# Performance work log

Measured on AMD Instinct MI355X. Metric: run time of the kernel, lower is better.

The kernel has to match this reference:

```python
import jax, jax.numpy as jnp
import numpy as np

B, T, E, D = 8, 2048, 1024, 128  # batch, seq, embedding_dim, head_dim


def setup_inputs() -> dict:
    key = jax.random.key(0)
    ks = jax.random.split(key, 7)
    s = 1.0 / np.sqrt(E)  # torch Linear default init scale
    return {
        "x": jax.random.normal(ks[0], (B, T, E), dtype=jnp.float32),
        "Wq": jax.random.uniform(ks[1], (E, D), jnp.float32, -s, s),
        "bq": jax.random.uniform(ks[2], (D,), jnp.float32, -s, s),
        "Wk": jax.random.uniform(ks[3], (E, D), jnp.float32, -s, s),
        "bk": jax.random.uniform(ks[4], (D,), jnp.float32, -s, s),
        "Wv": jax.random.uniform(ks[5], (E, D), jnp.float32, -s, s),
        "bv": jax.random.uniform(ks[6], (D,), jnp.float32, -s, s),
        "mask": 1,
    }


def reference(x, Wq, bq, Wk, bk, Wv, bv, mask):
    # Q/K/V projections: [B,T,E] @ [E,D] -> [B,T,D]
    q = x @ Wq + bq
    k = x @ Wk + bk
    v = x @ Wv + bv
    d_k = q.shape[-1]
    # scores: [B,T,T]
    scores = jnp.einsum("btd,bsd->bts", q, k) / jnp.sqrt(jnp.float32(d_k))
    if mask:  # causal masked_fill with -inf (static python flag)
        causal = jnp.tril(jnp.ones((q.shape[1], q.shape[1]), dtype=bool))
        scores = jnp.where(causal[None, :, :], scores, -jnp.inf)
    att = jax.nn.softmax(scores, axis=-1)
    # dropout p=0.0 (inference) -> identity
    return jnp.einsum("bts,bsd->btd", att, v)
```

## Files before the change

### kernel.cpp

```cpp
#include <hip/hip_runtime.h>
#include <hip/hip_bf16.h>

#define BSZ  8
#define TSEQ 2048
#define EDIM 1024
#define DDIM 128
#define MROWS (BSZ * TSEQ)
#define NQT  (TSEQ / 64)

typedef __attribute__((ext_vector_type(8))) __bf16 bf16x8;
typedef __attribute__((ext_vector_type(4))) __bf16 bf16x4;
typedef __attribute__((ext_vector_type(2))) __bf16 bf16x2;
typedef __attribute__((ext_vector_type(4))) float f32x4;

#define GLOAD_LDS(G, L) \
    __builtin_amdgcn_global_load_lds( \
        (const __attribute__((address_space(1))) void*)(G), \
        (__attribute__((address_space(3))) void*)(L), 16, 0, 0)

__global__ __launch_bounds__(256) void wt_kernel(
    const float* __restrict__ Wq, const float* __restrict__ Wk,
    const float* __restrict__ Wv, __bf16* __restrict__ wt)
{
    const float* W = (blockIdx.y == 0) ? Wq : (blockIdx.y == 1) ? Wk : Wv;
    __bf16* o = wt + (size_t)blockIdx.y * DDIM * EDIM;
    const int k0 = blockIdx.x * 64;
    __shared__ __align__(16) __bf16 t[64][140];
    const int tid = threadIdx.x;
    #pragma unroll
    for (int i = 0; i < 8; ++i) {
        int idx = tid + i * 256;
        int k = idx >> 5, c4 = idx & 31;
        float4 v = *(const float4*)&W[(size_t)(k0 + k) * DDIM + c4 * 4];
        bf16x4 b4;
        b4[0] = (__bf16)v.x; b4[1] = (__bf16)v.y; b4[2] = (__bf16)v.z; b4[3] = (__bf16)v.w;
        *(bf16x4*)&t[k][c4 * 4] = b4;
    }
    __syncthreads();
    #pragma unroll
    for (int i = 0; i < 4; ++i) {
        int idx = tid + i * 256;
        int n = idx >> 3, c8 = idx & 7;
        bf16x8 r;
        #pragma unroll
        for (int u = 0; u < 8; ++u) r[u] = t[c8 * 8 + u][n];
        *(bf16x8*)&o[(size_t)n * EDIM + k0 + c8 * 8] = r;
    }
}

#define A_LDS_BYTES 16384
#define B_LDS_BYTES 24576
#define BUF_BYTES   (A_LDS_BYTES + B_LDS_BYTES)

__global__ __launch_bounds__(256, 2) void qkv_fused_kernel(
    const float* __restrict__ x, const __bf16* __restrict__ wt,
    const float* __restrict__ bq, const float* __restrict__ bk,
    const float* __restrict__ bv,
    __bf16* __restrict__ qo, __bf16* __restrict__ ko, __bf16* __restrict__ vto)
{
    const int bid = blockIdx.x;
    const int xcd = bid & 7;
    const int nt  = (bid >> 3) & 1;
    const int mt  = (bid >> 4) * 8 + xcd;
    const int m0  = mt * 64;

    __shared__ __align__(16) char lds[2 * BUF_BYTES];

    const int tid  = threadIdx.x;
    const int lane = tid & 63;
    const int wv   = tid >> 6;
    const int wr   = wv >> 1, wc = wv & 1;
    const int cl   = lane & 15, gr = lane >> 4;

    f32x4 acc[2][6] = {};

    const float* asrc[4];
    int adst[4];
    #pragma unroll
    for (int i = 0; i < 4; ++i) {
        const int row  = i * 16 + (tid >> 4);
        const int lcol = ((tid & 15) * 16) ^ ((row & 7) << 4);
        asrc[i] = x + (size_t)(m0 + row) * EDIM + (lcol >> 2);
        adst[i] = i * 4096 + tid * 16;
    }
    const __bf16* bsrc[6];
    int bdst[6];
    #pragma unroll
    for (int i = 0; i < 6; ++i) {
        const int row  = i * 32 + (tid >> 3);
        const int lcol = ((tid & 7) * 16) ^ ((row & 7) << 4);
        bsrc[i] = wt + (size_t)(nt * 192 + row) * EDIM + (lcol >> 1);
        bdst[i] = A_LDS_BYTES + i * 4096 + tid * 16;
    }

    const int sw = (cl & 7) << 4;

#define STAGE(BUF, K0) do {                                                   \
    _Pragma("unroll")                                                         \
    for (int i = 0; i < 4; ++i)                                               \
        GLOAD_LDS(asrc[i] + (K0), lds + (BUF) * BUF_BYTES + adst[i]);         \
    _Pragma("unroll")                                                         \
    for (int i = 0; i < 6; ++i)                                               \
        GLOAD_LDS(bsrc[i] + (K0), lds + (BUF) * BUF_BYTES + bdst[i]);         \
  } while (0)

#define COMPUTE(BUF) do {                                                     \
    const char* base_ = lds + (BUF) * BUF_BYTES;                              \
    _Pragma("unroll")                                                         \
    for (int ks = 0; ks < 2; ++ks) {                                          \
        bf16x8 af[2], bfr[6];                                                 \
        _Pragma("unroll")                                                     \
        for (int mi = 0; mi < 2; ++mi) {                                      \
            const int ab = (wr * 32 + mi * 16 + cl) * 256 + ks * 128;         \
            f32x4 lo = *(const f32x4*)(base_ + ab + ((gr * 32)      ^ sw));   \
            f32x4 hi = *(const f32x4*)(base_ + ab + ((gr * 32 + 16) ^ sw));   \
            bf16x8 t;                                                         \
            t[0] = (__bf16)lo[0]; t[1] = (__bf16)lo[1];                       \
            t[2] = (__bf16)lo[2]; t[3] = (__bf16)lo[3];                       \
            t[4] = (__bf16)hi[0]; t[5] = (__bf16)hi[1];                       \
            t[6] = (__bf16)hi[2]; t[7] = (__bf16)hi[3];                       \
            af[mi] = t;                                                       \
        }                                                                     \
        _Pragma("unroll")                                                     \
        for (int ni = 0; ni < 6; ++ni) {                                      \
            const int off = A_LDS_BYTES + (wc * 96 + ni * 16 + cl) * 128      \
                          + ((ks * 64 + gr * 16) ^ sw);                       \
            bfr[ni] = *(const bf16x8*)(base_ + off);                          \
        }                                                                     \
        _Pragma("unroll")                                                     \
        for (int mi = 0; mi < 2; ++mi)                                        \
            _Pragma("unroll")                                                 \
            for (int ni = 0; ni < 6; ++ni)                                    \
                acc[mi][ni] = __builtin_amdgcn_mfma_f32_16x16x32_bf16(        \
                    af[mi], bfr[ni], acc[mi][ni], 0, 0, 0);                   \
    }                                                                         \
  } while (0)

    STAGE(0, 0);
    __syncthreads();

    #pragma unroll 1
    for (int k0 = 0; k0 < EDIM; k0 += 128) {
        STAGE(1, k0 + 64);
        COMPUTE(0);
        __syncthreads();
        if (k0 + 128 < EDIM) STAGE(0, k0 + 128);
        COMPUTE(1);
        __syncthreads();
    }
#undef STAGE
#undef COMPUTE

    const float qsc = 0.08838834764831845f;
    #pragma unroll
    for (int ni = 0; ni < 6; ++ni) {
        const int nbase = nt * 192 + wc * 96 + ni * 16;
        const int which = nbase >> 7;
        const int d     = (nbase & 127) + cl;
        const float* bias = (which == 0) ? bq : (which == 1) ? bk : bv;
        const float bb = bias[d];
        const float sc = (which == 0) ? qsc : 1.0f;
        #pragma unroll
        for (int mi = 0; mi < 2; ++mi) {
            const int row = m0 + wr * 32 + mi * 16 + gr * 4;
            if (which == 2) {
                bf16x4 p;
                #pragma unroll
                for (int r = 0; r < 4; ++r) p[r] = (__bf16)(acc[mi][ni][r] + bb);
                *(bf16x4*)&vto[(size_t)d * MROWS + row] = p;
            } else {
                __bf16* o = (which == 0) ? qo : ko;
                #pragma unroll
                for (int r = 0; r < 4; ++r)
                    o[(size_t)(row + r) * DDIM + d] = (__bf16)((acc[mi][ni][r] + bb) * sc);
            }
        }
    }
}

__global__ __launch_bounds__(256, 3) void attn_partial_kernel(
    const __bf16* __restrict__ Q, const __bf16* __restrict__ K,
    const __bf16* __restrict__ Vt,
    __bf16* __restrict__ partO, float* __restrict__ partM, float* __restrict__ partL,
    int PL, int NP)
{
    const int bid = blockIdx.x;
    const int b   = blockIdx.y;

    int g = 0, rem = bid;
    for (;;) {
        const int np_g = (g + 1 + PL - 1) / PL;
        if (rem < np_g) break;
        rem -= np_g; ++g;
    }
    const int qt = g, p = rem;
    const int tiles = qt + 1;
    const int np = (tiles + PL - 1) / PL;
    const int lb = tiles / np, ex = tiles % np;
    const int mylen = lb + (p < ex);
    const int start = p * lb + min(p, ex);
    const int kv_lo = start * 64;
    const int kv_hi = kv_lo + mylen * 64;

    __shared__ __align__(16) __bf16 k_lds[64][136];
    __shared__ __align__(16) __bf16 v_lds[128][72];
    __shared__ __align__(16) __bf16 p_lds[4][16][72];

    const int tid  = threadIdx.x;
    const int lane = tid & 63;
    const int w    = tid >> 6;
    const int cl   = lane & 15, gr = lane >> 4;

    const int qrow = qt * 64 + w * 16;
    const size_t bT = (size_t)b * TSEQ;

    bf16x8 qf[4];
    const __bf16* qbase = Q + (bT + qrow + cl) * DDIM;
    #pragma unroll
    for (int ks = 0; ks < 4; ++ks)
        qf[ks] = *(const bf16x8*)&qbase[ks * 32 + gr * 8];

    f32x4 acc[8] = {};
    float m1 = -__builtin_inff();
    float l1 = 0.f;

    bf16x8 rk[4], rv[4];
#define LOAD_TILE(KV0) do {                                                   \
    _Pragma("unroll")                                                         \
    for (int i = 0; i < 4; ++i) {                                             \
        int idx = tid + i * 256;                                              \
        rk[i] = *(const bf16x8*)&K[(bT + (KV0) + (idx >> 4)) * DDIM + (idx & 15) * 8]; } \
    _Pragma("unroll")                                                         \
    for (int i = 0; i < 4; ++i) {                                             \
        int idx = tid + i * 256;                                              \
        rv[i] = *(const bf16x8*)&Vt[(size_t)(idx >> 3) * MROWS + bT + (KV0) + (idx & 7) * 8]; } \
  } while (0)

    LOAD_TILE(kv_lo);

    for (int kv0 = kv_lo; kv0 < kv_hi; kv0 += 64) {
        #pragma unroll
        for (int i = 0; i < 4; ++i) {
            int idx = tid + i * 256;
            *(bf16x8*)&k_lds[idx >> 4][(idx & 15) * 8] = rk[i];
        }
        #pragma unroll
        for (int i = 0; i < 4; ++i) {
            int idx = tid + i * 256;
            *(bf16x8*)&v_lds[idx >> 3][(idx & 7) * 8] = rv[i];
        }
        __syncthreads();

        if (kv0 + 64 < kv_hi) LOAD_TILE(kv0 + 64);

        f32x4 s[4] = {};
        #pragma unroll
        for (int ks = 0; ks < 4; ++ks) {
            #pragma unroll
            for (int st = 0; st < 4; ++st) {
                bf16x8 kf = *(const bf16x8*)&k_lds[st * 16 + cl][ks * 32 + gr * 8];
                s[st] = __builtin_amdgcn_mfma_f32_16x16x32_bf16(kf, qf[ks], s[st], 0, 0, 0);
            }
        }

        if (kv0 + 63 > qrow) {
            const int kvb = kv0 + gr * 4 - qrow - cl;
            #pragma unroll
            for (int st = 0; st < 4; ++st)
                #pragma unroll
                for (int r = 0; r < 4; ++r)
                    if (kvb + st * 16 + r > 0) s[st][r] = -__builtin_inff();
        }

        float tm = fmaxf(fmaxf(fmaxf(s[0][0], s[0][1]), fmaxf(s[0][2], s[0][3])),
                         fmaxf(fmaxf(s[1][0], s[1][1]), fmaxf(s[1][2], s[1][3])));
        tm = fmaxf(tm,
             fmaxf(fmaxf(fmaxf(s[2][0], s[2][1]), fmaxf(s[2][2], s[2][3])),
                   fmaxf(fmaxf(s[3][0], s[3][1]), fmaxf(s[3][2], s[3][3]))));
        tm = fmaxf(tm, __shfl_xor(tm, 16));
        tm = fmaxf(tm, __shfl_xor(tm, 32));

        if (__any(tm > m1)) {
            const float newm = fmaxf(m1, tm);
            const float alpha = __expf(m1 - newm);
            l1 *= alpha;
            m1 = newm;
            float arec[4];
            #pragma unroll
            for (int r = 0; r < 4; ++r) arec[r] = __shfl(alpha, gr * 4 + r);
            #pragma unroll
            for (int d = 0; d < 8; ++d) {
                #pragma unroll
                for (int r = 0; r < 4; ++r) acc[d][r] *= arec[r];
            }
        }

        #pragma unroll
        for (int st = 0; st < 4; ++st) {
            #pragma unroll
            for (int u = 0; u < 2; ++u) {
                float p0 = __expf(s[st][2 * u]     - m1);
                float p1 = __expf(s[st][2 * u + 1] - m1);
                l1 += p0 + p1;
                bf16x2 pp; pp[0] = (__bf16)p0; pp[1] = (__bf16)p1;
                *(bf16x2*)&p_lds[w][cl][st * 16 + gr * 4 + 2 * u] = pp;
            }
        }

        #pragma unroll
        for (int ks2 = 0; ks2 < 2; ++ks2) {
            bf16x8 pa = *(const bf16x8*)&p_lds[w][cl][ks2 * 32 + gr * 8];
            #pragma unroll
            for (int d = 0; d < 8; ++d) {
                bf16x8 vf = *(const bf16x8*)&v_lds[d * 16 + cl][ks2 * 32 + gr * 8];
                acc[d] = __builtin_amdgcn_mfma_f32_16x16x32_bf16(pa, vf, acc[d], 0, 0, 0);
            }
        }
        __syncthreads();
    }
#undef LOAD_TILE

    const size_t pidx = (size_t)b * NP + bid;
    __bf16* po = partO + pidx * (64 * 128);
    float ls = l1;
    ls += __shfl_xor(ls, 16);
    ls += __shfl_xor(ls, 32);
    if (gr == 0) {
        partM[pidx * 64 + w * 16 + cl] = m1;
        partL[pidx * 64 + w * 16 + cl] = ls;
    }
    #pragma unroll
    for (int r = 0; r < 4; ++r) {
        const int row_l = w * 16 + gr * 4 + r;
        #pragma unroll
        for (int d = 0; d < 8; ++d)
            po[row_l * 128 + d * 16 + cl] = (__bf16)acc[d][r];
    }
}

__global__ __launch_bounds__(256) void attn_combine_kernel(
    const __bf16* __restrict__ partO, const float* __restrict__ partM,
    const float* __restrict__ partL, float* __restrict__ out, int PL, int NP)
{
    const int qt = blockIdx.x, b = blockIdx.y;
    int pre = 0;
    for (int g2 = 0; g2 < qt; ++g2) pre += (g2 + 1 + PL - 1) / PL;
    const int nv = (qt + 1 + PL - 1) / PL;
    const size_t pbase = (size_t)b * NP + pre;

    const int tid = threadIdx.x;
    const int col = (tid & 31) * 4;
    const int rbase = blockIdx.z * 32;

    #pragma unroll
    for (int rr = 0; rr < 4; ++rr) {
        const int row = rbase + (tid >> 5) + rr * 8;
        float mx = -__builtin_inff();
        for (int c = 0; c < nv; ++c)
            mx = fmaxf(mx, partM[(pbase + c) * 64 + row]);
        float lsum = 0.f;
        f32x4 o = {0.f, 0.f, 0.f, 0.f};
        for (int c = 0; c < nv; ++c) {
            const float wgt = __expf(partM[(pbase + c) * 64 + row] - mx);
            lsum += wgt * partL[(pbase + c) * 64 + row];
            const bf16x4 po = *(const bf16x4*)&partO[(pbase + c) * (64 * 128) + (size_t)row * 128 + col];
            o.x += wgt * (float)po[0]; o.y += wgt * (float)po[1];
            o.z += wgt * (float)po[2]; o.w += wgt * (float)po[3];
        }
        const float inv = 1.0f / lsum;
        f32x4 res = {o.x * inv, o.y * inv, o.z * inv, o.w * inv};
        *(f32x4*)&out[((size_t)b * TSEQ + qt * 64 + row) * DDIM + col] = res;
    }
}

extern "C" void kernel_launch(void* const* d_in, const int* in_sizes, int n_in,
                              void* d_out, int out_size, void* d_ws, size_t ws_size,
                              hipStream_t stream) {
    const float* x  = (const float*)d_in[0];
    const float* Wq = (const float*)d_in[1];
    const float* bq = (const float*)d_in[2];
    const float* Wk = (const float*)d_in[3];
    const float* bk = (const float*)d_in[4];
    const float* Wv = (const float*)d_in[5];
    const float* bv = (const float*)d_in[6];

    __bf16* q  = (__bf16*)d_ws;
    __bf16* k  = q  + (size_t)MROWS * DDIM;
    __bf16* vt = k  + (size_t)MROWS * DDIM;
    __bf16* wt = vt + (size_t)MROWS * DDIM;
    const size_t fixed_bytes = ((size_t)3 * MROWS * DDIM + (size_t)3 * DDIM * EDIM) * sizeof(__bf16);

    int PL = 4, NP = 0;
    for (int g2 = 0; g2 < NQT; ++g2) NP += (g2 + 1 + PL - 1) / PL;
    {
        const size_t need = fixed_bytes +
            (size_t)NP * BSZ * 64 * (128 * sizeof(__bf16) + 2 * sizeof(float));
        if (ws_size < need) {
            PL = 8; NP = 0;
            for (int g2 = 0; g2 < NQT; ++g2) NP += (g2 + 1 + PL - 1) / PL;
        }
    }
    __bf16* partO = (__bf16*)((char*)d_ws + fixed_bytes);
    float* partM = (float*)(partO + (size_t)NP * BSZ * 64 * 128);
    float* partL = partM + (size_t)NP * BSZ * 64;

    wt_kernel<<<dim3(EDIM / 64, 3), 256, 0, stream>>>(Wq, Wk, Wv, wt);
    qkv_fused_kernel<<<dim3(MROWS / 64 * 2), 256, 0, stream>>>(x, wt, bq, bk, bv, q, k, vt);
    attn_partial_kernel<<<dim3(NP, BSZ), 256, 0, stream>>>(q, k, vt, partO, partM, partL, PL, NP);
    attn_combine_kernel<<<dim3(NQT, BSZ, 2), 256, 0, stream>>>(partO, partM, partL,
                                                               (float*)d_out, PL, NP);
}
```

Measured before the change: 80.39 us.

## Double attention query tile to 128 rows and schedule heaviest splits first

Each attention block now handles 128 query rows, with each wave holding two 16-row Q fragments, so every K/V tile staged in LDS feeds twice as many MFMAs. This halves the K/V global and LDS traffic per query. The grid is flattened and reversed so the longest causal work items launch first, and batch is interleaved across neighbouring blocks. In exchange there are more registers per wave (launch bounds drop to 2 blocks per SIMD), fewer blocks, larger partial buffers, and -inf clamping in the softmax to avoid NaN on fully masked rows.

```diff
diff --git a/kernel.cpp b/kernel.cpp
--- a/kernel.cpp
+++ b/kernel.cpp
@@ -6,7 +6,7 @@
 #define EDIM 1024
 #define DDIM 128
 #define MROWS (BSZ * TSEQ)
-#define NQT  (TSEQ / 64)
+#define NQT2 (TSEQ / 128)
 
 typedef __attribute__((ext_vector_type(8))) __bf16 bf16x8;
 typedef __attribute__((ext_vector_type(4))) __bf16 bf16x4;
@@ -178,23 +178,23 @@
     }
 }
 
-__global__ __launch_bounds__(256, 3) void attn_partial_kernel(
+__global__ __launch_bounds__(256, 2) void attn_partial_kernel(
     const __bf16* __restrict__ Q, const __bf16* __restrict__ K,
     const __bf16* __restrict__ Vt,
     __bf16* __restrict__ partO, float* __restrict__ partM, float* __restrict__ partL,
     int PL, int NP)
 {
-    const int bid = blockIdx.x;
-    const int b   = blockIdx.y;
-
-    int g = 0, rem = bid;
+    const int b  = blockIdx.x & 7;
+    const int pc = NP - 1 - (blockIdx.x >> 3);
+
+    int g = 0, rem = pc;
     for (;;) {
-        const int np_g = (g + 1 + PL - 1) / PL;
+        const int np_g = (2 * g + 2 + PL - 1) / PL;
         if (rem < np_g) break;
         rem -= np_g; ++g;
     }
     const int qt = g, p = rem;
-    const int tiles = qt + 1;
+    const int tiles = 2 * qt + 2;
     const int np = (tiles + PL - 1) / PL;
     const int lb = tiles / np, ex = tiles % np;
     const int mylen = lb + (p < ex);
@@ -204,25 +204,28 @@
 
     __shared__ __align__(16) __bf16 k_lds[64][136];
     __shared__ __align__(16) __bf16 v_lds[128][72];
-    __shared__ __align__(16) __bf16 p_lds[4][16][72];
+    __shared__ __align__(16) __bf16 p_lds[4][2][16][72];
 
     const int tid  = threadIdx.x;
     const int lane = tid & 63;
     const int w    = tid >> 6;
     const int cl   = lane & 15, gr = lane >> 4;
 
-    const int qrow = qt * 64 + w * 16;
+    const int qrow = qt * 128 + w * 32;
     const size_t bT = (size_t)b * TSEQ;
 
-    bf16x8 qf[4];
-    const __bf16* qbase = Q + (bT + qrow + cl) * DDIM;
-    #pragma unroll
-    for (int ks = 0; ks < 4; ++ks)
-        qf[ks] = *(const bf16x8*)&qbase[ks * 32 + gr * 8];
-
-    f32x4 acc[8] = {};
-    float m1 = -__builtin_inff();
-    float l1 = 0.f;
+    bf16x8 qf[2][4];
+    #pragma unroll
+    for (int mi = 0; mi < 2; ++mi) {
+        const __bf16* qbase = Q + (bT + qrow + mi * 16 + cl) * DDIM;
+        #pragma unroll
+        for (int ks = 0; ks < 4; ++ks)
+            qf[mi][ks] = *(const bf16x8*)&qbase[ks * 32 + gr * 8];
+    }
+
+    f32x4 acc[2][8] = {};
+    float m1[2] = {-__builtin_inff(), -__builtin_inff()};
+    float l1[2] = {0.f, 0.f};
 
     bf16x8 rk[4], rv[4];
 #define LOAD_TILE(KV0) do {                                                   \
@@ -253,88 +256,108 @@
 
         if (kv0 + 64 < kv_hi) LOAD_TILE(kv0 + 64);
 
-        f32x4 s[4] = {};
+        f32x4 s[2][4] = {};
         #pragma unroll
         for (int ks = 0; ks < 4; ++ks) {
             #pragma unroll
             for (int st = 0; st < 4; ++st) {
                 bf16x8 kf = *(const bf16x8*)&k_lds[st * 16 + cl][ks * 32 + gr * 8];
-                s[st] = __builtin_amdgcn_mfma_f32_16x16x32_bf16(kf, qf[ks], s[st], 0, 0, 0);
+                s[0][st] = __builtin_amdgcn_mfma_f32_16x16x32_bf16(kf, qf[0][ks], s[0][st], 0, 0, 0);
+                s[1][st] = __builtin_amdgcn_mfma_f32_16x16x32_bf16(kf, qf[1][ks], s[1][st], 0, 0, 0);
             }
         }
 
         if (kv0 + 63 > qrow) {
-            const int kvb = kv0 + gr * 4 - qrow - cl;
-            #pragma unroll
-            for (int st = 0; st < 4; ++st)
-                #pragma unroll
-                for (int r = 0; r < 4; ++r)
-                    if (kvb + st * 16 + r > 0) s[st][r] = -__builtin_inff();
-        }
-
-        float tm = fmaxf(fmaxf(fmaxf(s[0][0], s[0][1]), fmaxf(s[0][2], s[0][3])),
-                         fmaxf(fmaxf(s[1][0], s[1][1]), fmaxf(s[1][2], s[1][3])));
-        tm = fmaxf(tm,
-             fmaxf(fmaxf(fmaxf(s[2][0], s[2][1]), fmaxf(s[2][2], s[2][3])),
-                   fmaxf(fmaxf(s[3][0], s[3][1]), fmaxf(s[3][2], s[3][3]))));
-        tm = fmaxf(tm, __shfl_xor(tm, 16));
-        tm = fmaxf(tm, __shfl_xor(tm, 32));
-
-        if (__any(tm > m1)) {
-            const float newm = fmaxf(m1, tm);
-            const float alpha = __expf(m1 - newm);
-            l1 *= alpha;
-            m1 = newm;
-            float arec[4];
-            #pragma unroll
-            for (int r = 0; r < 4; ++r) arec[r] = __shfl(alpha, gr * 4 + r);
-            #pragma unroll
-            for (int d = 0; d < 8; ++d) {
-                #pragma unroll
-                for (int r = 0; r < 4; ++r) acc[d][r] *= arec[r];
-            }
-        }
-
-        #pragma unroll
-        for (int st = 0; st < 4; ++st) {
-            #pragma unroll
-            for (int u = 0; u < 2; ++u) {
-                float p0 = __expf(s[st][2 * u]     - m1);
-                float p1 = __expf(s[st][2 * u + 1] - m1);
-                l1 += p0 + p1;
-                bf16x2 pp; pp[0] = (__bf16)p0; pp[1] = (__bf16)p1;
-                *(bf16x2*)&p_lds[w][cl][st * 16 + gr * 4 + 2 * u] = pp;
+            #pragma unroll
+            for (int mi = 0; mi < 2; ++mi) {
+                const int kvb = kv0 + gr * 4 - (qrow + mi * 16) - cl;
+                #pragma unroll
+                for (int st = 0; st < 4; ++st)
+                    #pragma unroll
+                    for (int r = 0; r < 4; ++r)
+                        if (kvb + st * 16 + r > 0) s[mi][st][r] = -__builtin_inff();
+            }
+        }
+
+        float tm[2];
+        #pragma unroll
+        for (int mi = 0; mi < 2; ++mi) {
+            float t0 = fmaxf(fmaxf(fmaxf(s[mi][0][0], s[mi][0][1]), fmaxf(s[mi][0][2], s[mi][0][3])),
+                             fmaxf(fmaxf(s[mi][1][0], s[mi][1][1]), fmaxf(s[mi][1][2], s[mi][1][3])));
+            t0 = fmaxf(t0,
+                 fmaxf(fmaxf(fmaxf(s[mi][2][0], s[mi][2][1]), fmaxf(s[mi][2][2], s[mi][2][3])),
+                       fmaxf(fmaxf(s[mi][3][0], s[mi][3][1]), fmaxf(s[mi][3][2], s[mi][3][3]))));
+            t0 = fmaxf(t0, __shfl_xor(t0, 16));
+            t0 = fmaxf(t0, __shfl_xor(t0, 32));
+            tm[mi] = t0;
+        }
+
+        if (__any((tm[0] > m1[0]) || (tm[1] > m1[1]))) {
+            #pragma unroll
+            for (int mi = 0; mi < 2; ++mi) {
+                const float newm = fmaxf(m1[mi], tm[mi]);
+                const float alpha = __expf(fmaxf(m1[mi], -3.0e38f) - fmaxf(newm, -3.0e38f));
+                l1[mi] *= alpha;
+                m1[mi] = newm;
+                float arec[4];
+                #pragma unroll
+                for (int r = 0; r < 4; ++r) arec[r] = __shfl(alpha, gr * 4 + r);
+                #pragma unroll
+                for (int d = 0; d < 8; ++d)
+                    #pragma unroll
+                    for (int r = 0; r < 4; ++r) acc[mi][d][r] *= arec[r];
+            }
+        }
+
+        #pragma unroll
+        for (int mi = 0; mi < 2; ++mi) {
+            const float mref = fmaxf(m1[mi], -3.0e38f);
+            #pragma unroll
+            for (int st = 0; st < 4; ++st) {
+                #pragma unroll
+                for (int u = 0; u < 2; ++u) {
+                    float p0 = __expf(s[mi][st][2 * u]     - mref);
+                    float p1 = __expf(s[mi][st][2 * u + 1] - mref);
+                    l1[mi] += p0 + p1;
+                    bf16x2 pp; pp[0] = (__bf16)p0; pp[1] = (__bf16)p1;
+                    *(bf16x2*)&p_lds[w][mi][cl][st * 16 + gr * 4 + 2 * u] = pp;
+                }
             }
         }
 
         #pragma unroll
         for (int ks2 = 0; ks2 < 2; ++ks2) {
-            bf16x8 pa = *(const bf16x8*)&p_lds[w][cl][ks2 * 32 + gr * 8];
+            bf16x8 pa0 = *(const bf16x8*)&p_lds[w][0][cl][ks2 * 32 + gr * 8];
+            bf16x8 pa1 = *(const bf16x8*)&p_lds[w][1][cl][ks2 * 32 + gr * 8];
             #pragma unroll
             for (int d = 0; d < 8; ++d) {
                 bf16x8 vf = *(const bf16x8*)&v_lds[d * 16 + cl][ks2 * 32 + gr * 8];
-                acc[d] = __builtin_amdgcn_mfma_f32_16x16x32_bf16(pa, vf, acc[d], 0, 0, 0);
+                acc[0][d] = __builtin_amdgcn_mfma_f32_16x16x32_bf16(pa0, vf, acc[0][d], 0, 0, 0);
+                acc[1][d] = __builtin_amdgcn_mfma_f32_16x16x32_bf16(pa1, vf, acc[1][d], 0, 0, 0);
             }
         }
         __syncthreads();
     }
 #undef LOAD_TILE
 
-    const size_t pidx = (size_t)b * NP + bid;
-    __bf16* po = partO + pidx * (64 * 128);
-    float ls = l1;
-    ls += __shfl_xor(ls, 16);
-    ls += __shfl_xor(ls, 32);
-    if (gr == 0) {
-        partM[pidx * 64 + w * 16 + cl] = m1;
-        partL[pidx * 64 + w * 16 + cl] = ls;
-    }
-    #pragma unroll
-    for (int r = 0; r < 4; ++r) {
-        const int row_l = w * 16 + gr * 4 + r;
-        #pragma unroll
-        for (int d = 0; d < 8; ++d)
-            po[row_l * 128 + d * 16 + cl] = (__bf16)acc[d][r];
+    const size_t pidx = (size_t)b * NP + pc;
+    __bf16* po = partO + pidx * (128 * 128);
+    #pragma unroll
+    for (int mi = 0; mi < 2; ++mi) {
+        float ls = l1[mi];
+        ls += __shfl_xor(ls, 16);
+        ls += __shfl_xor(ls, 32);
+        if (gr == 0) {
+            partM[pidx * 128 + w * 32 + mi * 16 + cl] = m1[mi];
+            partL[pidx * 128 + w * 32 + mi * 16 + cl] = ls;
+        }
+        #pragma unroll
+        for (int r = 0; r < 4; ++r) {
+            const int row_l = w * 32 + mi * 16 + gr * 4 + r;
+            #pragma unroll
+            for (int d = 0; d < 8; ++d)
+                po[row_l * 128 + d * 16 + cl] = (__bf16)acc[mi][d][r];
+        }
     }
 }
 
@@ -344,8 +367,8 @@
 {
     const int qt = blockIdx.x, b = blockIdx.y;
     int pre = 0;
-    for (int g2 = 0; g2 < qt; ++g2) pre += (g2 + 1 + PL - 1) / PL;
-    const int nv = (qt + 1 + PL - 1) / PL;
+    for (int g2 = 0; g2 < qt; ++g2) pre += (2 * g2 + 2 + PL - 1) / PL;
+    const int nv = (2 * qt + 2 + PL - 1) / PL;
     const size_t pbase = (size_t)b * NP + pre;
 
     const int tid = threadIdx.x;
@@ -357,19 +380,19 @@
         const int row = rbase + (tid >> 5) + rr * 8;
         float mx = -__builtin_inff();
         for (int c = 0; c < nv; ++c)
-            mx = fmaxf(mx, partM[(pbase + c) * 64 + row]);
+            mx = fmaxf(mx, partM[(pbase + c) * 128 + row]);
         float lsum = 0.f;
         f32x4 o = {0.f, 0.f, 0.f, 0.f};
         for (int c = 0; c < nv; ++c) {
-            const float wgt = __expf(partM[(pbase + c) * 64 + row] - mx);
-            lsum += wgt * partL[(pbase + c) * 64 + row];
-            const bf16x4 po = *(const bf16x4*)&partO[(pbase + c) * (64 * 128) + (size_t)row * 128 + col];
+            const float wgt = __expf(partM[(pbase + c) * 128 + row] - mx);
+            lsum += wgt * partL[(pbase + c) * 128 + row];
+            const bf16x4 po = *(const bf16x4*)&partO[(pbase + c) * (128 * 128) + (size_t)row * 128 + col];
             o.x += wgt * (float)po[0]; o.y += wgt * (float)po[1];
             o.z += wgt * (float)po[2]; o.w += wgt * (float)po[3];
         }
         const float inv = 1.0f / lsum;
         f32x4 res = {o.x * inv, o.y * inv, o.z * inv, o.w * inv};
-        *(f32x4*)&out[((size_t)b * TSEQ + qt * 64 + row) * DDIM + col] = res;
+        *(f32x4*)&out[((size_t)b * TSEQ + qt * 128 + row) * DDIM + col] = res;
     }
 }
 
@@ -391,22 +414,22 @@
     const size_t fixed_bytes = ((size_t)3 * MROWS * DDIM + (size_t)3 * DDIM * EDIM) * sizeof(__bf16);
 
     int PL = 4, NP = 0;
-    for (int g2 = 0; g2 < NQT; ++g2) NP += (g2 + 1 + PL - 1) / PL;
+    for (int g2 = 0; g2 < NQT2; ++g2) NP += (2 * g2 + 2 + PL - 1) / PL;
     {
         const size_t need = fixed_bytes +
-            (size_t)NP * BSZ * 64 * (128 * sizeof(__bf16) + 2 * sizeof(float));
+            (size_t)NP * BSZ * 128 * (128 * sizeof(__bf16) + 2 * sizeof(float));
         if (ws_size < need) {
             PL = 8; NP = 0;
-            for (int g2 = 0; g2 < NQT; ++g2) NP += (g2 + 1 + PL - 1) / PL;
+            for (int g2 = 0; g2 < NQT2; ++g2) NP += (2 * g2 + 2 + PL - 1) / PL;
         }
     }
     __bf16* partO = (__bf16*)((char*)d_ws + fixed_bytes);
-    float* partM = (float*)(partO + (size_t)NP * BSZ * 64 * 128);
-    float* partL = partM + (size_t)NP * BSZ * 64;
+    float* partM = (float*)(partO + (size_t)NP * BSZ * 128 * 128);
+    float* partL = partM + (size_t)NP * BSZ * 128;
 
     wt_kernel<<<dim3(EDIM / 64, 3), 256, 0, stream>>>(Wq, Wk, Wv, wt);
     qkv_fused_kernel<<<dim3(MROWS / 64 * 2), 256, 0, stream>>>(x, wt, bq, bk, bv, q, k, vt);
-    attn_partial_kernel<<<dim3(NP, BSZ), 256, 0, stream>>>(q, k, vt, partO, partM, partL, PL, NP);
-    attn_combine_kernel<<<dim3(NQT, BSZ, 2), 256, 0, stream>>>(partO, partM, partL,
-                                                               (float*)d_out, PL, NP);
+    attn_partial_kernel<<<dim3(NP * BSZ), 256, 0, stream>>>(q, k, vt, partO, partM, partL, PL, NP);
+    attn_combine_kernel<<<dim3(NQT2, BSZ, 4), 256, 0, stream>>>(partO, partM, partL,
+                                                                (float*)d_out, PL, NP);
 }
```

Result: slower. 98.84 us (+23.0%).
